# Performance work log

Hardware: AMD Instinct MI355X
Metric: run time of the kernel (lower is better)

Reference implementation:

```python
import jax, jax.numpy as jnp
from jax import lax
import numpy as np

B, C, L = 32, 8, 512
C_IN = 512      # must equal L (tokenConv consumes permuted tensor)
D_MODEL = 512
SCALE_NUM = 64  # 63 actual scales


def build_wavelet_bank(scale_num, LB=-8.0, UB=8.0, N=1024, Fb=2.0, Fc=8.0):
    """Replicates cmor_torch; returns centered zero-padded kernel bank [S, K].
    Zero-centering is exact because every kernel length (16*s+1) is odd and K is odd,
    so the padded conv with pad=(K-1)//2 equals the original per-scale conv with
    pad=(k-1)//2."""
    x = np.linspace(LB, UB, N)
    wav = (np.pi * Fb) ** (-0.5) * np.exp(2j * np.pi * Fc * x) * np.exp(-x ** 2 / Fb)
    step = x[1] - x[0]
    kernels = []
    for scale in np.arange(1, scale_num):
        j = (np.arange(scale * (x[-1] - x[0]) + 1) / (scale * step)).astype(int)
        j = j[j < wav.size]
        kernels.append(np.real(wav[j]) * scale ** (-0.5))
    K = max(len(k) for k in kernels)
    if K % 2 == 0:
        K += 1
    bank = np.zeros((len(kernels), K), np.float32)
    for i, k in enumerate(kernels):
        assert (K - len(k)) % 2 == 0, "kernel parity mismatch"
        off = (K - len(k)) // 2
        bank[i, off:off + len(k)] = k
    return bank


def setup_inputs() -> dict:
    key = jax.random.key(0)
    k1, k2 = jax.random.split(key)
    x = jax.random.normal(k1, (B, C, L), dtype=jnp.float32)
    wavelet_bank = jnp.asarray(build_wavelet_bank(SCALE_NUM))  # [63, K]
    token_w = jax.random.normal(k2, (D_MODEL, C_IN, 3), dtype=jnp.float32) * 0.02
    return {"x": x, "wavelet_bank": wavelet_bank, "token_w": token_w}


def reference(x, wavelet_bank, token_w):
    Bb, Cc, Ll = x.shape
    S, K = wavelet_bank.shape
    pad = (K - 1) // 2
    # fused CWT over all (channel, scale) pairs: [B*C, 1, L] conv [S, 1, K] -> [B*C, S, L]
    xr = x.reshape(Bb * Cc, 1, Ll)
    conv = lax.conv_general_dilated(
        xr, wavelet_bank[:, None, :], window_strides=(1,),
        padding=[(pad, pad)], dimension_numbers=("NCH", "OIH", "NCH"))
    d = jnp.abs(jnp.diff(conv, axis=-1))                 # [B*C, S, L-1]
    d = jnp.concatenate([d, d[..., -1:]], axis=-1)       # replicate last sample -> L
    feats = d.reshape(Bb, Cc * S, Ll)
    out = jnp.concatenate([x, feats], axis=1)            # [B, C*(1+S), L]
    # tokenConv on permuted tensor: channels = L (= c_in), length = C*(1+S)
    h = out.transpose(0, 2, 1)                           # [B, L, C_total]
    hp = jnp.concatenate([h[..., -1:], h, h[..., :1]], axis=-1)  # circular pad=1
    y = lax.conv_general_dilated(
        hp, token_w, window_strides=(1,), padding="VALID",
        dimension_numbers=("NCH", "OIH", "NCH"))         # [B, d_model, C_total]
    return y.transpose(0, 2, 1)                          # [B, C_total, d_model]
```

## Files before the change

### kernel.cpp

```cpp
#include <hip/hip_runtime.h>
#include <hip/hip_bf16.h>

#define NB 32
#define NC 8
#define NL 512
#define NS 63
#define NK 1009
#define NPAD 504
#define ND 512
#define NCT 512
#define NROWS 514

typedef __attribute__((ext_vector_type(4))) float f32x4;
typedef __attribute__((ext_vector_type(8))) short short8;
typedef __attribute__((ext_vector_type(4))) short short4v;

#define APAD_BYTES (NB * NROWS * NL * 2)
#define WB_BYTES   (3 * ND * NL * 2)
#define BANKB_BYTES (64 * 1024 * 2)

typedef const __attribute__((address_space(1))) unsigned int* gp1_t;
typedef __attribute__((address_space(3))) unsigned int* lp3_t;
__device__ __forceinline__ void gload_lds16(const void* g, void* l) {
  __builtin_amdgcn_global_load_lds((gp1_t)g, (lp3_t)l, 16, 0, 0);
}

__device__ __forceinline__ unsigned short bf16_bits(float v) {
  return __builtin_bit_cast(unsigned short, __float2bfloat16(v));
}

#define WAITVM(N) asm volatile("s_waitcnt vmcnt(" #N ")" ::: "memory")
#define FENCE() asm volatile("" ::: "memory")
#define BAR() __builtin_amdgcn_s_barrier()
#define PRIO1() __builtin_amdgcn_s_setprio(1)
#define PRIO0() __builtin_amdgcn_s_setprio(0)

__global__ __launch_bounds__(256) void prep_kernel(
    const float* __restrict__ bank, const float* __restrict__ tw,
    __hip_bfloat16* __restrict__ Wb, __hip_bfloat16* __restrict__ bankB) {
  const int idx = blockIdx.x * 256 + threadIdx.x;

  {
    int i0 = idx * 4;
    const float4* t4 = (const float4*)(tw + (size_t)i0 * 3);
    float4 a = t4[0], bq = t4[1], c4 = t4[2];
    ushort4 w0 = make_ushort4(bf16_bits(a.x), bf16_bits(a.w), bf16_bits(bq.z), bf16_bits(c4.y));
    ushort4 w1 = make_ushort4(bf16_bits(a.y), bf16_bits(bq.x), bf16_bits(bq.w), bf16_bits(c4.z));
    ushort4 w2 = make_ushort4(bf16_bits(a.z), bf16_bits(bq.y), bf16_bits(c4.x), bf16_bits(c4.w));
    *(ushort4*)(Wb + 0 * ND * NL + i0) = w0;
    *(ushort4*)(Wb + 1 * ND * NL + i0) = w1;
    *(ushort4*)(Wb + 2 * ND * NL + i0) = w2;
  }
  {
    int s = idx >> 10, k = idx & 1023;
    float v = (s < NS && k < NK) ? bank[s * NK + k] : 0.f;
    bankB[idx] = __float2bfloat16(v);
  }
}

#define CPY_STRIDE 3088

__global__ __launch_bounds__(512) void cwt_kernel(
    const float* __restrict__ x, const __hip_bfloat16* __restrict__ bankB,
    __hip_bfloat16* __restrict__ Apad) {
  __shared__ char smem[8 * 16384 + 4 * CPY_STRIDE];
  char* bankS = smem;
  char* cpy = smem + 8 * 16384;

  const int tid = threadIdx.x;
  const int bc = blockIdx.x;
  const int b = bc >> 3, c = bc & 7;
  const int w = tid >> 6, l = tid & 63;
  const int hi = l >> 4, li = l & 15;

  const float* xrow = x + bc * NL;

  if (tid < 512) {
    __hip_bfloat16 v = __float2bfloat16(xrow[tid]);
    Apad[((size_t)(b * NROWS) + 1 + c) * NL + tid] = v;
    if (c == 0) Apad[((size_t)(b * NROWS) + 513) * NL + tid] = v;
  }

  for (int i = 0; i < 6; ++i) {
    int p = tid + i * 512;
    int r_ = p / 768, pe = p - r_ * 768;
    int e0 = 2 * pe;
    int i0 = e0 + r_;
    float xa = (i0 >= NPAD && i0 < NPAD + NL) ? xrow[i0 - NPAD] : 0.f;
    float xb = (i0 + 1 >= NPAD && i0 + 1 < NPAD + NL) ? xrow[i0 + 1 - NPAD] : 0.f;
    float xc = (i0 + 2 >= NPAD && i0 + 2 < NPAD + NL) ? xrow[i0 + 2 - NPAD] : 0.f;
    unsigned short u0 = bf16_bits(xb - xa);
    unsigned short u1 = bf16_bits(xc - xb);
    *(unsigned int*)(cpy + r_ * CPY_STRIDE + e0 * 2) = (unsigned)u0 | ((unsigned)u1 << 16);
  }

#define STAGE(kt)                                                             \
  {                                                                           \
    for (int i = 0; i < 2; ++i) {                                             \
      int ck = tid + i * 512;                                                 \
      int s_ = ck >> 4, rb = ck & 15;                                         \
      int srcc = rb ^ (s_ & 7);                                               \
      gload_lds16(bankB + s_ * 1024 + (kt) * 128 + srcc * 8,                  \
                  bankS + (kt) * 16384 + ck * 16);                            \
    }                                                                         \
  }

#define AVMM(kt, ksl, m)                                                       \
  {                                                                            \
    int srow = (m) * 16 + li;                                                  \
    int chunk = ((ksl) * 4 + hi) ^ (srow & 7);                                 \
    short8 av = *(const short8*)(bankS + (kt) * 16384 + srow * 256 + chunk * 16); \
    _Pragma("unroll") for (int n = 0; n < 4; ++n)                              \
      acc[m][n] = __builtin_amdgcn_mfma_f32_16x16x32_bf16(av, bv[n],           \
                                                          acc[m][n], 0, 0, 0); \
  }

#define CCOMP(kt, M0, M1, M2, M3)                                              \
  {                                                                            \
    _Pragma("unroll") for (int ksl = 0; ksl < 4; ++ksl) {                      \
      short8 bv[4];                                                            \
      _Pragma("unroll") for (int n = 0; n < 4; ++n) {                          \
        int t = tbase + n * 16 + li;                                           \
        int e = t - r + (kt) * 128 + ksl * 32 + hi * 8;                        \
        const char* pc = cpy + r * CPY_STRIDE + e * 2;                         \
        short4v lo = *(const short4v*)pc;                                      \
        short4v hh = *(const short4v*)(pc + 8);                                \
        short8 f;                                                              \
        f[0] = lo[0]; f[1] = lo[1]; f[2] = lo[2]; f[3] = lo[3];                \
        f[4] = hh[0]; f[5] = hh[1]; f[6] = hh[2]; f[7] = hh[3];                \
        bv[n] = f;                                                             \
      }                                                                        \
      PRIO1();                                                                 \
      if (M0) AVMM(kt, ksl, 0);                                                \
      if (M1) AVMM(kt, ksl, 1);                                                \
      if (M2) AVMM(kt, ksl, 2);                                                \
      if (M3) AVMM(kt, ksl, 3);                                                \
      PRIO0();                                                                 \
    }                                                                          \
  }

  STAGE(0); STAGE(1); STAGE(2); STAGE(3);
  STAGE(4); STAGE(5); STAGE(6); STAGE(7);

  f32x4 acc[4][4] = {};
  const int r = l & 3;
  const int tbase = w * 64;

  asm volatile("s_waitcnt vmcnt(14) lgkmcnt(0)" ::: "memory");
  BAR(); FENCE(); CCOMP(0, 0, 0, 1, 1);
  WAITVM(12); BAR(); FENCE(); CCOMP(1, 0, 1, 1, 1);
  WAITVM(10); BAR(); FENCE(); CCOMP(2, 1, 1, 1, 1);
  WAITVM(8);  BAR(); FENCE(); CCOMP(3, 1, 1, 1, 1);
  WAITVM(6);  BAR(); FENCE(); CCOMP(4, 1, 1, 1, 1);
  WAITVM(4);  BAR(); FENCE(); CCOMP(5, 0, 1, 1, 1);
  WAITVM(2);  BAR(); FENCE(); CCOMP(6, 0, 0, 1, 1);
  WAITVM(0);  BAR(); FENCE(); CCOMP(7, 0, 0, 0, 1);

#pragma unroll
  for (int m = 0; m < 4; ++m) {
#pragma unroll
    for (int rg = 0; rg < 4; ++rg) {
      int s = m * 16 + hi * 4 + rg;
      if (s >= NS) continue;
      int ch = 8 + c * NS + s;
      size_t rowbase = ((size_t)(b * NROWS) + 1 + ch) * NL;
#pragma unroll
      for (int n = 0; n < 4; ++n) {
        int t = tbase + n * 16 + li;
        float d = fabsf(acc[m][n][rg]);
        __hip_bfloat16 hv = __float2bfloat16(d);
        bool lastgrp = (w == 7 && n == 3);
        bool skip = lastgrp && (li == 15);
        bool dup = lastgrp && (li == 14);
        if (!skip) Apad[rowbase + t] = hv;
        if (dup) Apad[rowbase + 511] = hv;
        if (ch == NCT - 1) {
          size_t wrapbase = (size_t)(b * NROWS) * NL;
          if (!skip) Apad[wrapbase + t] = hv;
          if (dup) Apad[wrapbase + 511] = hv;
        }
      }
    }
  }
#undef STAGE
#undef AVMM
#undef CCOMP
}

__global__ __launch_bounds__(256) void gemm_kernel(
    const __hip_bfloat16* __restrict__ Ap, const __hip_bfloat16* __restrict__ Wb,
    float* __restrict__ out) {
  __shared__ __hip_bfloat16 sA[5][128 * 32];
  __shared__ __hip_bfloat16 sB[5][128 * 32];

  const int tid = threadIdx.x;
  const int gid = blockIdx.x;
  const int q = gid >> 3;
  const int pid = (gid & 7) * 16 + (q >> 2);
  const int b = pid >> 2;
  const int p0 = (pid & 3) * 128;
  const int o0 = (q & 3) * 128;

  const int w = tid >> 6, lane = tid & 63;
  const int wm = w >> 1, wn = w & 1;
  const int row_in = lane & 15, hi = lane >> 4;

  const int r0 = tid >> 2, cg0 = (tid & 3) ^ ((r0 >> 1) & 3);
  const int ck1 = tid + 256;
  const int r1 = ck1 >> 2, cg1 = (ck1 & 3) ^ ((r1 >> 1) & 3);

#define GSTAGE(kk, bu)                                                         \
  {                                                                            \
    const int kap_ = (kk) >> 4;                                                \
    const int l0_ = ((kk) & 15) << 5;                                          \
    gload_lds16(Ap + ((b * NROWS + p0 + kap_ + r0) * NL + l0_ + cg0 * 8),      \
                &sA[bu][tid * 8]);                                             \
    gload_lds16(Ap + ((b * NROWS + p0 + kap_ + r1) * NL + l0_ + cg1 * 8),      \
                &sA[bu][ck1 * 8]);                                             \
    gload_lds16(Wb + ((kap_ * ND + o0 + r0) * NL + l0_ + cg0 * 8),             \
                &sB[bu][tid * 8]);                                             \
    gload_lds16(Wb + ((kap_ * ND + o0 + r1) * NL + l0_ + cg1 * 8),             \
                &sB[bu][ck1 * 8]);                                             \
  }

#define COMPUTE(bu)                                                            \
  {                                                                            \
    short8 av[4], bv[4];                                                       \
    _Pragma("unroll") for (int m = 0; m < 4; ++m) {                            \
      int row = wm * 64 + m * 16 + row_in;                                     \
      int slot = row * 4 + (hi ^ ((row >> 1) & 3));                            \
      av[m] = *(const short8*)(&sA[bu][slot * 8]);                             \
    }                                                                          \
    _Pragma("unroll") for (int n = 0; n < 4; ++n) {                            \
      int row = wn * 64 + n * 16 + row_in;                                     \
      int slot = row * 4 + (hi ^ ((row >> 1) & 3));                            \
      bv[n] = *(const short8*)(&sB[bu][slot * 8]);                             \
    }                                                                          \
    PRIO1();                                                                   \
    _Pragma("unroll") for (int m = 0; m < 4; ++m)                              \
      _Pragma("unroll") for (int n = 0; n < 4; ++n)                            \
        acc[m][n] = __builtin_amdgcn_mfma_f32_16x16x32_bf16(av[m], bv[n],      \
                                                            acc[m][n], 0, 0, 0); \
    PRIO0();                                                                   \
  }

#define STEP(kk, bu, bs)                                                       \
  GSTAGE((kk) + 3, bs); WAITVM(12); BAR(); FENCE(); COMPUTE(bu); FENCE();

  f32x4 acc[4][4] = {};

  GSTAGE(0, 0); GSTAGE(1, 1); GSTAGE(2, 2);

  for (int g = 0; g < 9; ++g) {
    const int kk = g * 5;
    STEP(kk + 0, 0, 3);
    STEP(kk + 1, 1, 4);
    STEP(kk + 2, 2, 0);
    STEP(kk + 3, 3, 1);
    STEP(kk + 4, 4, 2);
  }
  WAITVM(8); BAR(); FENCE(); COMPUTE(0); FENCE();
  WAITVM(4); BAR(); FENCE(); COMPUTE(1); FENCE();
  WAITVM(0); BAR(); FENCE(); COMPUTE(2);
#undef GSTAGE
#undef COMPUTE
#undef STEP

#pragma unroll
  for (int m = 0; m < 4; ++m) {
    const int p = p0 + wm * 64 + m * 16 + hi * 4;
#pragma unroll
    for (int n = 0; n < 4; ++n) {
      const int o = o0 + wn * 64 + n * 16 + row_in;
#pragma unroll
      for (int r = 0; r < 4; ++r)
        out[(size_t)((b * NCT) + p + r) * ND + o] = acc[m][n][r];
    }
  }
}

extern "C" void kernel_launch(void* const* d_in, const int* in_sizes, int n_in,
                              void* d_out, int out_size, void* d_ws, size_t ws_size,
                              hipStream_t stream) {
  const float* x = (const float*)d_in[0];
  const float* bank = (const float*)d_in[1];
  const float* tw = (const float*)d_in[2];
  float* out = (float*)d_out;

  char* ws = (char*)d_ws;
  __hip_bfloat16* Apad = (__hip_bfloat16*)ws;
  __hip_bfloat16* Wb = (__hip_bfloat16*)(ws + APAD_BYTES);
  __hip_bfloat16* bankB = (__hip_bfloat16*)(ws + APAD_BYTES + WB_BYTES);

  prep_kernel<<<256, 256, 0, stream>>>(bank, tw, Wb, bankB);
  cwt_kernel<<<256, 512, 0, stream>>>(x, bankB, Apad);
  gemm_kernel<<<512, 256, 0, stream>>>(Apad, Wb, out);
}
```

Baseline: 66.25 us.

## Split CWT blocks in half, read bank and GEMM A-operand directly from global

The CWT kernel now launches twice as many 256-thread blocks, each computing half the time positions. The wavelet bank is read straight from global memory instead of being staged through LDS with a pipelined wait schedule. In the GEMM, the A operand is loaded from global into registers and double-buffered across steps, so only B is staged in LDS, which cuts LDS use and barrier traffic. Priority hints are removed throughout. The costs are more global/L2 traffic for the repeated bank and A reads, loss of the explicit load/compute overlap in the CWT kernel, and uncoalesced per-lane 16-byte global loads for A.

```diff
diff --git a/kernel.cpp b/kernel.cpp
--- a/kernel.cpp
+++ b/kernel.cpp
@@ -17,7 +17,6 @@
 
 #define APAD_BYTES (NB * NROWS * NL * 2)
 #define WB_BYTES   (3 * ND * NL * 2)
-#define BANKB_BYTES (64 * 1024 * 2)
 
 typedef const __attribute__((address_space(1))) unsigned int* gp1_t;
 typedef __attribute__((address_space(3))) unsigned int* lp3_t;
@@ -32,8 +31,6 @@
 #define WAITVM(N) asm volatile("s_waitcnt vmcnt(" #N ")" ::: "memory")
 #define FENCE() asm volatile("" ::: "memory")
 #define BAR() __builtin_amdgcn_s_barrier()
-#define PRIO1() __builtin_amdgcn_s_setprio(1)
-#define PRIO0() __builtin_amdgcn_s_setprio(0)
 
 __global__ __launch_bounds__(256) void prep_kernel(
     const float* __restrict__ bank, const float* __restrict__ tw,
@@ -60,56 +57,51 @@
 
 #define CPY_STRIDE 3088
 
-__global__ __launch_bounds__(512) void cwt_kernel(
+__global__ __launch_bounds__(256) void cwt_kernel(
     const float* __restrict__ x, const __hip_bfloat16* __restrict__ bankB,
     __hip_bfloat16* __restrict__ Apad) {
-  __shared__ char smem[8 * 16384 + 4 * CPY_STRIDE];
-  char* bankS = smem;
-  char* cpy = smem + 8 * 16384;
+  __shared__ char cpy[4 * CPY_STRIDE];
 
   const int tid = threadIdx.x;
-  const int bc = blockIdx.x;
+  const int gid = blockIdx.x;
+  const int bc = gid >> 1, half = gid & 1;
   const int b = bc >> 3, c = bc & 7;
   const int w = tid >> 6, l = tid & 63;
   const int hi = l >> 4, li = l & 15;
 
   const float* xrow = x + bc * NL;
 
-  if (tid < 512) {
-    __hip_bfloat16 v = __float2bfloat16(xrow[tid]);
-    Apad[((size_t)(b * NROWS) + 1 + c) * NL + tid] = v;
-    if (c == 0) Apad[((size_t)(b * NROWS) + 513) * NL + tid] = v;
-  }
-
-  for (int i = 0; i < 6; ++i) {
-    int p = tid + i * 512;
-    int r_ = p / 768, pe = p - r_ * 768;
-    int e0 = 2 * pe;
-    int i0 = e0 + r_;
-    float xa = (i0 >= NPAD && i0 < NPAD + NL) ? xrow[i0 - NPAD] : 0.f;
-    float xb = (i0 + 1 >= NPAD && i0 + 1 < NPAD + NL) ? xrow[i0 + 1 - NPAD] : 0.f;
-    float xc = (i0 + 2 >= NPAD && i0 + 2 < NPAD + NL) ? xrow[i0 + 2 - NPAD] : 0.f;
-    unsigned short u0 = bf16_bits(xb - xa);
-    unsigned short u1 = bf16_bits(xc - xb);
-    *(unsigned int*)(cpy + r_ * CPY_STRIDE + e0 * 2) = (unsigned)u0 | ((unsigned)u1 << 16);
-  }
-
-#define STAGE(kt)                                                             \
-  {                                                                           \
-    for (int i = 0; i < 2; ++i) {                                             \
-      int ck = tid + i * 512;                                                 \
-      int s_ = ck >> 4, rb = ck & 15;                                         \
-      int srcc = rb ^ (s_ & 7);                                               \
-      gload_lds16(bankB + s_ * 1024 + (kt) * 128 + srcc * 8,                  \
-                  bankS + (kt) * 16384 + ck * 16);                            \
-    }                                                                         \
-  }
+  {
+    int t = half * 256 + tid;
+    __hip_bfloat16 v = __float2bfloat16(xrow[t]);
+    Apad[((size_t)(b * NROWS) + 1 + c) * NL + t] = v;
+    if (c == 0) Apad[((size_t)(b * NROWS) + 513) * NL + t] = v;
+  }
+
+  const int pebase = half ? 112 : 0;
+  for (int i = 0; i < 11; ++i) {
+    int j = tid + i * 256;
+    int r_ = (j >> 6) / 11;
+    int pe = pebase + (j - r_ * 704);
+    if (pe < 768) {
+      int e0 = 2 * pe, i0 = e0 + r_;
+      float xa = (i0 >= NPAD && i0 < NPAD + NL) ? xrow[i0 - NPAD] : 0.f;
+      float xb = (i0 + 1 >= NPAD && i0 + 1 < NPAD + NL) ? xrow[i0 + 1 - NPAD] : 0.f;
+      float xc = (i0 + 2 >= NPAD && i0 + 2 < NPAD + NL) ? xrow[i0 + 2 - NPAD] : 0.f;
+      unsigned u = (unsigned)bf16_bits(xb - xa) | ((unsigned)bf16_bits(xc - xb) << 16);
+      *(unsigned*)(cpy + r_ * CPY_STRIDE + e0 * 2) = u;
+    }
+  }
+  __syncthreads();
+
+  f32x4 acc[4][4] = {};
+  const int r = l & 3;
+  const int tbase = (half * 4 + w) * 64;
 
 #define AVMM(kt, ksl, m)                                                       \
   {                                                                            \
-    int srow = (m) * 16 + li;                                                  \
-    int chunk = ((ksl) * 4 + hi) ^ (srow & 7);                                 \
-    short8 av = *(const short8*)(bankS + (kt) * 16384 + srow * 256 + chunk * 16); \
+    const short8 av = *(const short8*)(bankB + ((m) * 16 + li) * 1024 +        \
+                                       (kt) * 128 + (ksl) * 32 + hi * 8);      \
     _Pragma("unroll") for (int n = 0; n < 4; ++n)                              \
       acc[m][n] = __builtin_amdgcn_mfma_f32_16x16x32_bf16(av, bv[n],           \
                                                           acc[m][n], 0, 0, 0); \
@@ -123,38 +115,26 @@
         int t = tbase + n * 16 + li;                                           \
         int e = t - r + (kt) * 128 + ksl * 32 + hi * 8;                        \
         const char* pc = cpy + r * CPY_STRIDE + e * 2;                         \
-        short4v lo = *(const short4v*)pc;                                      \
-        short4v hh = *(const short4v*)(pc + 8);                                \
         short8 f;                                                              \
-        f[0] = lo[0]; f[1] = lo[1]; f[2] = lo[2]; f[3] = lo[3];                \
-        f[4] = hh[0]; f[5] = hh[1]; f[6] = hh[2]; f[7] = hh[3];                \
+        *(short4v*)&f = *(const short4v*)pc;                                   \
+        *(((short4v*)&f) + 1) = *(const short4v*)(pc + 8);                     \
         bv[n] = f;                                                             \
       }                                                                        \
-      PRIO1();                                                                 \
       if (M0) AVMM(kt, ksl, 0);                                                \
       if (M1) AVMM(kt, ksl, 1);                                                \
       if (M2) AVMM(kt, ksl, 2);                                                \
       if (M3) AVMM(kt, ksl, 3);                                                \
-      PRIO0();                                                                 \
     }                                                                          \
   }
 
-  STAGE(0); STAGE(1); STAGE(2); STAGE(3);
-  STAGE(4); STAGE(5); STAGE(6); STAGE(7);
-
-  f32x4 acc[4][4] = {};
-  const int r = l & 3;
-  const int tbase = w * 64;
-
-  asm volatile("s_waitcnt vmcnt(14) lgkmcnt(0)" ::: "memory");
-  BAR(); FENCE(); CCOMP(0, 0, 0, 1, 1);
-  WAITVM(12); BAR(); FENCE(); CCOMP(1, 0, 1, 1, 1);
-  WAITVM(10); BAR(); FENCE(); CCOMP(2, 1, 1, 1, 1);
-  WAITVM(8);  BAR(); FENCE(); CCOMP(3, 1, 1, 1, 1);
-  WAITVM(6);  BAR(); FENCE(); CCOMP(4, 1, 1, 1, 1);
-  WAITVM(4);  BAR(); FENCE(); CCOMP(5, 0, 1, 1, 1);
-  WAITVM(2);  BAR(); FENCE(); CCOMP(6, 0, 0, 1, 1);
-  WAITVM(0);  BAR(); FENCE(); CCOMP(7, 0, 0, 0, 1);
+  CCOMP(0, 0, 0, 1, 1);
+  CCOMP(1, 0, 1, 1, 1);
+  CCOMP(2, 1, 1, 1, 1);
+  CCOMP(3, 1, 1, 1, 1);
+  CCOMP(4, 1, 1, 1, 1);
+  CCOMP(5, 0, 1, 1, 1);
+  CCOMP(6, 0, 0, 1, 1);
+  CCOMP(7, 0, 0, 0, 1);
 
 #pragma unroll
   for (int m = 0; m < 4; ++m) {
@@ -169,7 +149,7 @@
         int t = tbase + n * 16 + li;
         float d = fabsf(acc[m][n][rg]);
         __hip_bfloat16 hv = __float2bfloat16(d);
-        bool lastgrp = (w == 7 && n == 3);
+        bool lastgrp = (tbase + n * 16 == 496);
         bool skip = lastgrp && (li == 15);
         bool dup = lastgrp && (li == 14);
         if (!skip) Apad[rowbase + t] = hv;
@@ -182,7 +162,6 @@
       }
     }
   }
-#undef STAGE
 #undef AVMM
 #undef CCOMP
 }
@@ -190,7 +169,6 @@
 __global__ __launch_bounds__(256) void gemm_kernel(
     const __hip_bfloat16* __restrict__ Ap, const __hip_bfloat16* __restrict__ Wb,
     float* __restrict__ out) {
-  __shared__ __hip_bfloat16 sA[5][128 * 32];
   __shared__ __hip_bfloat16 sB[5][128 * 32];
 
   const int tid = threadIdx.x;
@@ -209,60 +187,65 @@
   const int ck1 = tid + 256;
   const int r1 = ck1 >> 2, cg1 = (ck1 & 3) ^ ((r1 >> 1) & 3);
 
-#define GSTAGE(kk, bu)                                                         \
+#define BSTAGE(kk, bu)                                                         \
   {                                                                            \
     const int kap_ = (kk) >> 4;                                                \
     const int l0_ = ((kk) & 15) << 5;                                          \
-    gload_lds16(Ap + ((b * NROWS + p0 + kap_ + r0) * NL + l0_ + cg0 * 8),      \
-                &sA[bu][tid * 8]);                                             \
-    gload_lds16(Ap + ((b * NROWS + p0 + kap_ + r1) * NL + l0_ + cg1 * 8),      \
-                &sA[bu][ck1 * 8]);                                             \
     gload_lds16(Wb + ((kap_ * ND + o0 + r0) * NL + l0_ + cg0 * 8),             \
                 &sB[bu][tid * 8]);                                             \
     gload_lds16(Wb + ((kap_ * ND + o0 + r1) * NL + l0_ + cg1 * 8),             \
                 &sB[bu][ck1 * 8]);                                             \
   }
 
-#define COMPUTE(bu)                                                            \
-  {                                                                            \
-    short8 av[4], bv[4];                                                       \
-    _Pragma("unroll") for (int m = 0; m < 4; ++m) {                            \
-      int row = wm * 64 + m * 16 + row_in;                                     \
-      int slot = row * 4 + (hi ^ ((row >> 1) & 3));                            \
-      av[m] = *(const short8*)(&sA[bu][slot * 8]);                             \
-    }                                                                          \
+#define ALOAD(kk, AV)                                                          \
+  {                                                                            \
+    const int kap_ = (kk) >> 4;                                                \
+    const int l0_ = ((kk) & 15) << 5;                                          \
+    _Pragma("unroll") for (int m = 0; m < 4; ++m)                              \
+      AV[m] = *(const short8*)(Ap +                                            \
+          ((size_t)(b * NROWS) + p0 + kap_ + wm * 64 + m * 16 + row_in) * NL + \
+          l0_ + hi * 8);                                                       \
+  }
+
+#define COMPUTE(bu, AV)                                                        \
+  {                                                                            \
+    short8 bv[4];                                                              \
     _Pragma("unroll") for (int n = 0; n < 4; ++n) {                            \
       int row = wn * 64 + n * 16 + row_in;                                     \
       int slot = row * 4 + (hi ^ ((row >> 1) & 3));                            \
       bv[n] = *(const short8*)(&sB[bu][slot * 8]);                             \
     }                                                                          \
-    PRIO1();                                                                   \
     _Pragma("unroll") for (int m = 0; m < 4; ++m)                              \
       _Pragma("unroll") for (int n = 0; n < 4; ++n)                            \
-        acc[m][n] = __builtin_amdgcn_mfma_f32_16x16x32_bf16(av[m], bv[n],      \
+        acc[m][n] = __builtin_amdgcn_mfma_f32_16x16x32_bf16(AV[m], bv[n],      \
                                                             acc[m][n], 0, 0, 0); \
-    PRIO0();                                                                   \
-  }
-
-#define STEP(kk, bu, bs)                                                       \
-  GSTAGE((kk) + 3, bs); WAITVM(12); BAR(); FENCE(); COMPUTE(bu); FENCE();
+  }
+
+#define STEP(kk, CUR, NXT)                                                     \
+  ALOAD((kk) + 1, NXT); FENCE();                                               \
+  BSTAGE((kk) + 3, ((kk) + 3) % 5);                                            \
+  WAITVM(8); BAR(); FENCE();                                                   \
+  COMPUTE((kk) % 5, CUR); FENCE();
 
   f32x4 acc[4][4] = {};
-
-  GSTAGE(0, 0); GSTAGE(1, 1); GSTAGE(2, 2);
-
-  for (int g = 0; g < 9; ++g) {
-    const int kk = g * 5;
-    STEP(kk + 0, 0, 3);
-    STEP(kk + 1, 1, 4);
-    STEP(kk + 2, 2, 0);
-    STEP(kk + 3, 3, 1);
-    STEP(kk + 4, 4, 2);
-  }
-  WAITVM(8); BAR(); FENCE(); COMPUTE(0); FENCE();
-  WAITVM(4); BAR(); FENCE(); COMPUTE(1); FENCE();
-  WAITVM(0); BAR(); FENCE(); COMPUTE(2);
-#undef GSTAGE
+  short8 avA[4], avB[4];
+
+  ALOAD(0, avA); FENCE();
+  BSTAGE(0, 0); BSTAGE(1, 1); BSTAGE(2, 2);
+
+#pragma unroll
+  for (int kp = 0; kp < 22; ++kp) {
+    STEP(2 * kp, avA, avB);
+    STEP(2 * kp + 1, avB, avA);
+  }
+  STEP(44, avA, avB);
+  ALOAD(46, avA); FENCE();
+  WAITVM(6); BAR(); FENCE(); COMPUTE(0, avB); FENCE();
+  ALOAD(47, avB); FENCE();
+  WAITVM(4); BAR(); FENCE(); COMPUTE(1, avA); FENCE();
+  WAITVM(0); BAR(); FENCE(); COMPUTE(2, avB);
+#undef BSTAGE
+#undef ALOAD
 #undef COMPUTE
 #undef STEP
 
@@ -293,6 +276,6 @@
   __hip_bfloat16* bankB = (__hip_bfloat16*)(ws + APAD_BYTES + WB_BYTES);
 
   prep_kernel<<<256, 256, 0, stream>>>(bank, tw, Wb, bankB);
-  cwt_kernel<<<256, 512, 0, stream>>>(x, bankB, Apad);
+  cwt_kernel<<<512, 256, 0, stream>>>(x, bankB, Apad);
   gemm_kernel<<<512, 256, 0, stream>>>(Apad, Wb, out);
 }
```

Measured after the change: 102.8 us. +55.1%, slower.
